# Kernel tuning notes

Hardware: AMD Instinct MI355X
Metric: run time of the kernel (lower is better)

The kernel has to match this reference:

```python
import jax, jax.numpy as jnp
import numpy as np

HEADS, DIM_HEAD = 8, 64
SCALE = DIM_HEAD ** -0.5
LAMDA1, LAMDA2 = 5.0, 5.0


def setup_inputs() -> dict:
    B, N, M = 32, 1536, 80  # N = 32*48 spatial tokens, M = max_boxes
    QD, KD, VD = 320, 768, 768
    inner = HEADS * DIM_HEAD
    ks = jax.random.split(jax.random.key(0), 11)
    return {
        "x": jax.random.normal(ks[0], (B, N, QD), jnp.float32),
        "key": jax.random.normal(ks[1], (B, M, KD), jnp.float32),
        "value": jax.random.normal(ks[2], (B, M, VD), jnp.float32),
        "mask": jax.random.randint(ks[3], (B, M), 0, 2).astype(bool),
        "perl_box_masking_map": jax.random.normal(ks[4], (B, N, M), jnp.float32),
        "perl_road_masking_map": jax.random.normal(ks[5], (B, 1, N), jnp.float32),
        "Wq": jax.random.normal(ks[6], (inner, QD), jnp.float32) * 0.02,
        "Wk": jax.random.normal(ks[7], (inner, KD), jnp.float32) * 0.02,
        "Wv": jax.random.normal(ks[8], (inner, VD), jnp.float32) * 0.02,
        "Wo": jax.random.normal(ks[9], (QD, inner), jnp.float32) * 0.02,
        "bo": jnp.zeros((QD,), jnp.float32),
    }


def reference(x, key, value, mask, perl_box_masking_map, perl_road_masking_map, Wq, Wk, Wv, Wo, bo):
    B, N, _ = x.shape
    M = key.shape[1]
    H, C = HEADS, DIM_HEAD
    # QKV projections (torch Linear: y = x @ W.T)
    q = (x @ Wq.T).reshape(B, N, H, C)
    k = (key @ Wk.T).reshape(B, M, H, C)
    v = (value @ Wv.T).reshape(B, M, H, C)
    # attention scores with scale, key mask, and two additive bias maps
    sim = jnp.einsum('bnhc,bmhc->bhnm', q, k) * SCALE  # (B, H, N, M)
    neg = -jnp.finfo(sim.dtype).max
    sim = jnp.where(mask[:, None, None, :], sim, neg)  # mask fill BEFORE bias adds, as in torch
    sim = sim + LAMDA1 * perl_box_masking_map[:, None, :, :]
    road = jnp.swapaxes(perl_road_masking_map, 1, 2)  # (B, N, 1) -> broadcast over key axis
    sim = sim + LAMDA2 * road[:, None, :, :]
    attn = jax.nn.softmax(sim, axis=-1)
    out = jnp.einsum('bhnm,bmhc->bnhc', attn, v).reshape(B, N, H * C)
    return out @ Wo.T + bo  # dropout is identity in eval
```

## Files before the change

### kernel.cpp

```cpp
#include <hip/hip_runtime.h>
#include <hip/hip_bf16.h>

typedef __attribute__((ext_vector_type(8))) short short8;
typedef __attribute__((ext_vector_type(4))) short short4v;
typedef __attribute__((ext_vector_type(4))) float floatx4;
typedef unsigned short u16;

#define NB 32
#define NN 1536
#define NM 80
#define NH 8
#define NC 64
#define NINNER 512
#define NQD 320
#define NKD 768

__device__ __forceinline__ float bf2f(u16 u) {
    union { unsigned i; float f; } x; x.i = ((unsigned)u) << 16; return x.f;
}
__device__ __forceinline__ u16 f2bf(float f) {
    unsigned u = __float_as_uint(f);
    unsigned r = (u + 0x7FFFu + ((u >> 16) & 1u)) >> 16;
    return (u16)r;
}
__device__ __forceinline__ short8 cvt8(const float* __restrict__ p) {
    float4 a = ((const float4*)p)[0];
    float4 b = ((const float4*)p)[1];
    short8 r;
    r[0] = (short)f2bf(a.x); r[1] = (short)f2bf(a.y);
    r[2] = (short)f2bf(a.z); r[3] = (short)f2bf(a.w);
    r[4] = (short)f2bf(b.x); r[5] = (short)f2bf(b.y);
    r[6] = (short)f2bf(b.z); r[7] = (short)f2bf(b.w);
    return r;
}
__device__ __forceinline__ void gload16(const u16* g, u16* l) {
    __builtin_amdgcn_global_load_lds(
        (const __attribute__((address_space(1))) unsigned int*)g,
        (__attribute__((address_space(3))) unsigned int*)l, 16, 0, 0);
}

__global__ __launch_bounds__(256) void prep(const u16* __restrict__ x,
                                            const unsigned char* __restrict__ raw,
                                            int* __restrict__ flag,
                                            float* __restrict__ maskbias) {
    if (blockIdx.x == 0) {
        __shared__ int cnt;
        if (threadIdx.x == 0) cnt = 0;
        __syncthreads();
        int c = 0;
        for (int i = threadIdx.x; i < 8192; i += 256) {
            unsigned e = (x[i] >> 7) & 0xFF;
            if (e >= 0xA0) c++;
        }
        atomicAdd(&cnt, c);
        __syncthreads();
        if (threadIdx.x == 0) *flag = (cnt > 64) ? 1 : 0;
    } else {
        __shared__ int c_bf, c_f32, c_u8;
        if (threadIdx.x == 0) { c_bf = 0; c_f32 = 0; c_u8 = 0; }
        __syncthreads();
        for (int i = threadIdx.x; i < NB * NM; i += 256) {
            unsigned char v = raw[i];
            if (v == 0x3F && (i & 3) == 1) atomicAdd(&c_bf, 1);
            if (v == 0x3F && (i & 3) == 3) atomicAdd(&c_f32, 1);
            if (v != 0 && (i & 3) != 0) atomicAdd(&c_u8, 1);
        }
        __syncthreads();
        int md;
        if (c_bf > 0) md = 2;
        else if (c_f32 > 0) md = 3;
        else if (c_u8 > 0) md = 1;
        else md = 0;
        for (int i = threadIdx.x; i < NB * NM; i += 256) {
            bool on;
            if (md == 2) on = ((const u16*)raw)[i] != 0;
            else if (md == 3) on = ((const float*)raw)[i] != 0.0f;
            else if (md == 1) on = raw[i] != 0;
            else on = ((const int*)raw)[i] != 0;
            maskbias[i] = on ? 0.0f : -3.4028234663852886e38f;
        }
    }
}

struct ConvSeg { const void* src; u16* dst; long nreal; long nblk; };
struct ConvArgs { ConvSeg s[7]; };

__global__ __launch_bounds__(256) void conv_batch(ConvArgs a, const int* __restrict__ flag) {
    const int f = *flag;
    long b = blockIdx.x; int seg = 0;
    while (seg < 7 && b >= a.s[seg].nblk) { b -= a.s[seg].nblk; seg++; }
    if (seg >= 7) return;
    const long idx = b * 2048 + threadIdx.x * 8;
    u16* dst = a.s[seg].dst;
    if (idx >= a.s[seg].nreal) { *(short8*)(dst + idx) = (short8)0; return; }
    if (f) *(short8*)(dst + idx) = cvt8((const float*)a.s[seg].src + idx);
    else   *(short8*)(dst + idx) = *(const short8*)((const u16*)a.s[seg].src + idx);
}

template <bool OUT_DYN, bool BIAS>
__device__ __forceinline__ void gemm_body(const u16* __restrict__ A,
                                          const u16* __restrict__ B,
                                          const void* __restrict__ bias,
                                          void* __restrict__ C,
                                          int bx, int by, int Nreal, int K, int f,
                                          u16* As, u16* Bs) {
    const int tid = threadIdx.x;
    const int wave = tid >> 6, lane = tid & 63;
    const int l16 = lane & 15, quad = lane >> 4;
    const int wr = wave >> 1, wc = wave & 1;
    const int bm0 = bx * 128, bn0 = by * 128;

    const int r0 = tid >> 2, c0 = tid & 3;
    const int sc = c0 ^ ((r0 >> 1) & 3);
    const u16* Ag = A + (size_t)(bm0 + r0) * K + sc * 8;
    const u16* Bg = B + (size_t)(bn0 + r0) * K + sc * 8;
    u16* AsW = As + wave * 512;
    u16* BsW = Bs + wave * 512;

    const int swz = (l16 >> 1) & 3;
    floatx4 acc[4][4];
#pragma unroll
    for (int i = 0; i < 4; ++i)
#pragma unroll
        for (int n = 0; n < 4; ++n) acc[i][n] = (floatx4)0.0f;

    for (int kk = 0; kk < K; kk += 32) {
        __syncthreads();
#pragma unroll
        for (int j = 0; j < 2; ++j) {
            gload16(Ag + (size_t)(j * 64) * K + kk, AsW + j * 2048);
            gload16(Bg + (size_t)(j * 64) * K + kk, BsW + j * 2048);
        }
        __syncthreads();
        short8 af[4], bf[4];
#pragma unroll
        for (int i = 0; i < 4; ++i)
            af[i] = *(const short8*)&As[(wr * 64 + i * 16 + l16) * 32 + ((quad ^ swz) * 8)];
#pragma unroll
        for (int n = 0; n < 4; ++n)
            bf[n] = *(const short8*)&Bs[(wc * 64 + n * 16 + l16) * 32 + ((quad ^ swz) * 8)];
#pragma unroll
        for (int i = 0; i < 4; ++i)
#pragma unroll
            for (int n = 0; n < 4; ++n)
                acc[i][n] = __builtin_amdgcn_mfma_f32_16x16x32_bf16(af[i], bf[n], acc[i][n], 0, 0, 0);
    }

#pragma unroll
    for (int n = 0; n < 4; ++n) {
        const int col = bn0 + wc * 64 + n * 16 + l16;
        if (col < Nreal) {
            float badd = 0.0f;
            if (BIAS) badd = f ? ((const float*)bias)[col] : bf2f(((const u16*)bias)[col]);
#pragma unroll
            for (int i = 0; i < 4; ++i)
#pragma unroll
                for (int r = 0; r < 4; ++r) {
                    const int row = bm0 + wr * 64 + i * 16 + quad * 4 + r;
                    const float val = acc[i][n][r] + badd;
                    if (OUT_DYN && f) ((float*)C)[(size_t)row * Nreal + col] = val;
                    else              ((u16*)C)[(size_t)row * Nreal + col] = f2bf(val);
                }
        }
    }
}

struct GemmRoles {
    const u16* A[3]; const u16* B[3]; u16* C[3];
    int mblk[3]; int kdim[3]; int start[3];
};

__global__ __launch_bounds__(256) void gemm_qkv(GemmRoles g) {
    __shared__ __align__(16) u16 As[128 * 32];
    __shared__ __align__(16) u16 Bs[128 * 32];
    const int id = blockIdx.x;
    const int role = (id >= g.start[1]) + (id >= g.start[2]);
    const int rid = id - g.start[role];
    const int mb = g.mblk[role];
    const int bx = rid % mb, by = rid / mb;
    gemm_body<false, false>(g.A[role], g.B[role], nullptr, g.C[role],
                            bx, by, NINNER, g.kdim[role], 0, As, Bs);
}

__global__ __launch_bounds__(256) void gemm_out(const u16* __restrict__ A,
                                                const u16* __restrict__ B,
                                                const void* __restrict__ bias,
                                                void* __restrict__ C,
                                                const int* __restrict__ flag) {
    __shared__ __align__(16) u16 As[128 * 32];
    __shared__ __align__(16) u16 Bs[128 * 32];
    const int f = *flag;
    gemm_body<true, true>(A, B, bias, C, blockIdx.x, blockIdx.y, NQD, NINNER, f, As, Bs);
}

__global__ __launch_bounds__(256) void transpose_v(const u16* __restrict__ v,
                                                   u16* __restrict__ vT) {
    int b = blockIdx.x >> 3, h = blockIdx.x & 7;
    const u16* src = v + (size_t)b * NM * NINNER + h * NC;
    u16* o = vT + (size_t)(b * NH + h) * NC * 96;
    for (int idx = threadIdx.x; idx < NM * NC; idx += 256) {
        int m = idx >> 6, c = idx & 63;
        o[c * 96 + m] = src[(size_t)m * NINNER + c];
    }
    for (int idx = threadIdx.x; idx < NC * 16; idx += 256) {
        int c = idx >> 4, m = 80 + (idx & 15);
        o[c * 96 + m] = 0;
    }
}

__global__ __launch_bounds__(256) void attn_kernel(const u16* __restrict__ q,
                                                   const u16* __restrict__ k,
                                                   const u16* __restrict__ vT,
                                                   const float* __restrict__ maskbias,
                                                   const void* __restrict__ box,
                                                   const void* __restrict__ road,
                                                   u16* __restrict__ attno,
                                                   const int* __restrict__ flag) {
    const int f = *flag;
    const int n0 = blockIdx.x * 64;
    const int h = blockIdx.y;
    const int b = blockIdx.z;
    const int tid = threadIdx.x;
    const int wave = tid >> 6, lane = tid & 63;
    const int l16 = lane & 15, quad = lane >> 4;

    __shared__ __align__(16) u16 p_lds[64][104];

    const int n = n0 + 16 * wave + l16;
    const size_t qrow = (size_t)(b * NN + n) * NINNER + h * NC;
    short8 qa[2];
    qa[0] = *(const short8*)(q + qrow + 0 + quad * 8);
    qa[1] = *(const short8*)(q + qrow + 32 + quad * 8);
    short8 kf[5][2];
#pragma unroll
    for (int mt = 0; mt < 5; ++mt) {
        const u16* kr = k + (size_t)(b * NM + mt * 16 + l16) * NINNER + h * NC + quad * 8;
        kf[mt][0] = *(const short8*)(kr + 0);
        kf[mt][1] = *(const short8*)(kr + 32);
    }
    const size_t boxbase = ((size_t)b * NN + n) * NM;
    floatx4 bx4[5]; short4v bxh[5]; floatx4 mb4[5];
    float roadf = 0.0f; u16 roadh = 0;
    if (f) {
#pragma unroll
        for (int mt = 0; mt < 5; ++mt)
            bx4[mt] = *(const floatx4*)((const float*)box + boxbase + 16 * mt + 4 * quad);
        roadf = ((const float*)road)[(size_t)b * NN + n];
    } else {
#pragma unroll
        for (int mt = 0; mt < 5; ++mt)
            bxh[mt] = *(const short4v*)((const u16*)box + boxbase + 16 * mt + 4 * quad);
        roadh = ((const u16*)road)[(size_t)b * NN + n];
    }
#pragma unroll
    for (int mt = 0; mt < 5; ++mt)
        mb4[mt] = *(const floatx4*)(maskbias + b * NM + 16 * mt + 4 * quad);

    floatx4 s[5];
#pragma unroll
    for (int i = 0; i < 5; ++i) s[i] = (floatx4)0.0f;
#pragma unroll
    for (int kk2 = 0; kk2 < 2; ++kk2)
#pragma unroll
        for (int mt = 0; mt < 5; ++mt)
            s[mt] = __builtin_amdgcn_mfma_f32_16x16x32_bf16(kf[mt][kk2], qa[kk2], s[mt], 0, 0, 0);

    const float roadv = 5.0f * (f ? roadf : bf2f(roadh));
#pragma unroll
    for (int mt = 0; mt < 5; ++mt)
#pragma unroll
        for (int r = 0; r < 4; ++r) {
            const float boxv = 5.0f * (f ? bx4[mt][r] : bf2f((u16)bxh[mt][r]));
            s[mt][r] = s[mt][r] * 0.125f + mb4[mt][r] + boxv + roadv;
        }

    float mx = s[0][0];
#pragma unroll
    for (int mt = 0; mt < 5; ++mt) {
        float t = fmaxf(fmaxf(s[mt][0], s[mt][1]), fmaxf(s[mt][2], s[mt][3]));
        mx = (mt == 0) ? t : fmaxf(mx, t);
    }
    mx = fmaxf(mx, __shfl_xor(mx, 16));
    mx = fmaxf(mx, __shfl_xor(mx, 32));
    float sum = 0.0f;
#pragma unroll
    for (int mt = 0; mt < 5; ++mt)
#pragma unroll
        for (int r = 0; r < 4; ++r) {
            const float p = __expf(s[mt][r] - mx);
            s[mt][r] = p;
            sum += p;
        }
    sum += __shfl_xor(sum, 16);
    sum += __shfl_xor(sum, 32);
    const float inv = 1.0f / sum;

#pragma unroll
    for (int mt = 0; mt < 5; ++mt) {
        short4v pk;
#pragma unroll
        for (int r = 0; r < 4; ++r) pk[r] = (short)f2bf(s[mt][r] * inv);
        *(short4v*)&p_lds[16 * wave + l16][16 * mt + 4 * quad] = pk;
    }
    if (quad < 2) *(short8*)&p_lds[16 * wave + l16][80 + 8 * quad] = (short8)0;
    asm volatile("s_waitcnt lgkmcnt(0)" ::: "memory");
    __builtin_amdgcn_sched_barrier(0);

    floatx4 o[4];
#pragma unroll
    for (int i = 0; i < 4; ++i) o[i] = (floatx4)0.0f;
    const u16* vbase = vT + (size_t)(b * NH + h) * NC * 96;
#pragma unroll
    for (int kk = 0; kk < 96; kk += 32) {
        short8 a = *(const short8*)&p_lds[16 * wave + l16][kk + quad * 8];
#pragma unroll
        for (int nt = 0; nt < 4; ++nt) {
            short8 bf = *(const short8*)(vbase + (size_t)(nt * 16 + l16) * 96 + kk + quad * 8);
            o[nt] = __builtin_amdgcn_mfma_f32_16x16x32_bf16(a, bf, o[nt], 0, 0, 0);
        }
    }

#pragma unroll
    for (int nt = 0; nt < 4; ++nt) {
#pragma unroll
        for (int r = 0; r < 4; ++r) {
            int nr = n0 + 16 * wave + quad * 4 + r;
            attno[((size_t)b * NN + nr) * NINNER + h * NC + nt * 16 + l16] = f2bf(o[nt][r]);
        }
    }
}

extern "C" void kernel_launch(void* const* d_in, const int* in_sizes, int n_in,
                              void* d_out, int out_size, void* d_ws, size_t ws_size,
                              hipStream_t stream) {
    (void)in_sizes; (void)n_in; (void)out_size; (void)ws_size;
    const void* x    = d_in[0];
    const void* key  = d_in[1];
    const void* val  = d_in[2];
    const unsigned char* mask = (const unsigned char*)d_in[3];
    const void* box  = d_in[4];
    const void* road = d_in[5];
    const void* Wq   = d_in[6];
    const void* Wk   = d_in[7];
    const void* Wv   = d_in[8];
    const void* Wo   = d_in[9];
    const void* bo   = d_in[10];

    char* ws = (char*)d_ws;
    size_t off = 0;
    auto carve = [&](size_t bytes) {
        char* p = ws + off;
        off += (bytes + 255) & ~(size_t)255;
        return p;
    };
    int* flag   = (int*)carve(256);
    u16* q_ws   = (u16*)carve((size_t)NB * NN * NINNER * 2);
    u16* k_ws   = (u16*)carve((size_t)NB * NM * NINNER * 2);
    u16* v_ws   = (u16*)carve((size_t)NB * NM * NINNER * 2);
    u16* vT_ws  = (u16*)carve((size_t)NB * NH * NC * 96 * 2);
    u16* ao_ws  = (u16*)carve((size_t)NB * NN * NINNER * 2);
    u16* x_bf   = ao_ws;
    u16* key_bf = (u16*)carve((size_t)NB * NM * NKD * 2);
    u16* val_bf = (u16*)carve((size_t)NB * NM * NKD * 2);
    u16* Wq_bf  = (u16*)carve((size_t)NINNER * NQD * 2);
    u16* Wk_bf  = (u16*)carve((size_t)NINNER * NKD * 2);
    u16* Wv_bf  = (u16*)carve((size_t)NINNER * NKD * 2);
    u16* WoP_bf = (u16*)carve((size_t)384 * NINNER * 2);
    float* mb   = (float*)carve((size_t)NB * NM * 4);

    prep<<<2, 256, 0, stream>>>((const u16*)x, mask, flag, mb);

    ConvArgs ca;
    ca.s[0] = { x,     x_bf,   (long)NB * NN * NQD, (long)NB * NN * NQD / 2048 };
    ca.s[1] = { key,   key_bf, (long)NB * NM * NKD, (long)NB * NM * NKD / 2048 };
    ca.s[2] = { val,   val_bf, (long)NB * NM * NKD, (long)NB * NM * NKD / 2048 };
    ca.s[3] = { Wq,    Wq_bf,  (long)NINNER * NQD,  (long)NINNER * NQD / 2048 };
    ca.s[4] = { Wk,    Wk_bf,  (long)NINNER * NKD,  (long)NINNER * NKD / 2048 };
    ca.s[5] = { Wv,    Wv_bf,  (long)NINNER * NKD,  (long)NINNER * NKD / 2048 };
    ca.s[6] = { Wo,    WoP_bf, (long)NQD * NINNER,  (long)384 * NINNER / 2048 };
    long totblk = 0;
    for (int i = 0; i < 7; ++i) totblk += ca.s[i].nblk;
    conv_batch<<<(int)totblk, 256, 0, stream>>>(ca, flag);

    GemmRoles g;
    g.A[0] = key_bf; g.B[0] = Wk_bf; g.C[0] = k_ws; g.mblk[0] = NB * NM / 128; g.kdim[0] = NKD;
    g.A[1] = val_bf; g.B[1] = Wv_bf; g.C[1] = v_ws; g.mblk[1] = NB * NM / 128; g.kdim[1] = NKD;
    g.A[2] = x_bf;   g.B[2] = Wq_bf; g.C[2] = q_ws; g.mblk[2] = NB * NN / 128; g.kdim[2] = NQD;
    g.start[0] = 0;
    g.start[1] = g.mblk[0] * 4;
    g.start[2] = g.start[1] + g.mblk[1] * 4;
    int gtot = g.start[2] + g.mblk[2] * 4;
    gemm_qkv<<<gtot, 256, 0, stream>>>(g);

    transpose_v<<<NB * NH, 256, 0, stream>>>(v_ws, vT_ws);
    attn_kernel<<<dim3(NN / 64, NH, NB), 256, 0, stream>>>(
        q_ws, k_ws, vT_ws, mb, box, road, ao_ws, flag);
    gemm_out<<<dim3(NB * NN / 128, 384 / 128), 256, 0, stream>>>(
        ao_ws, WoP_bf, bo, d_out, flag);
}
```

Baseline: 324.0 us.

## Double-buffer GEMM LDS tiles and prefetch V fragments in attention kernel

The shared GEMM body now double-buffers its A/B LDS tiles, issuing the next K-slice's global-to-LDS loads before computing on the current slice. This leaves one barrier per iteration instead of two. In the attention kernel, V fragments are loaded into registers right after the QK MFMAs so their latency overlaps the softmax. The bias sum, max reduction and bf16 packing via v_cvt_pk_bf16_f32 are also restructured. LDS usage per GEMM block doubles, and the prefetched V fragments raise register pressure.

```diff
diff --git a/kernel.cpp b/kernel.cpp
--- a/kernel.cpp
+++ b/kernel.cpp
@@ -4,6 +4,7 @@
 typedef __attribute__((ext_vector_type(8))) short short8;
 typedef __attribute__((ext_vector_type(4))) short short4v;
 typedef __attribute__((ext_vector_type(4))) float floatx4;
+typedef __attribute__((ext_vector_type(2))) unsigned uint2v;
 typedef unsigned short u16;
 
 #define NB 32
@@ -22,6 +23,11 @@
     unsigned u = __float_as_uint(f);
     unsigned r = (u + 0x7FFFu + ((u >> 16) & 1u)) >> 16;
     return (u16)r;
+}
+__device__ __forceinline__ unsigned cvt_pk_bf16(float lo, float hi) {
+    unsigned r;
+    asm("v_cvt_pk_bf16_f32 %0, %1, %2" : "=v"(r) : "v"(lo), "v"(hi));
+    return r;
 }
 __device__ __forceinline__ short8 cvt8(const float* __restrict__ p) {
     float4 a = ((const float4*)p)[0];
@@ -114,8 +120,6 @@
     const int sc = c0 ^ ((r0 >> 1) & 3);
     const u16* Ag = A + (size_t)(bm0 + r0) * K + sc * 8;
     const u16* Bg = B + (size_t)(bn0 + r0) * K + sc * 8;
-    u16* AsW = As + wave * 512;
-    u16* BsW = Bs + wave * 512;
 
     const int swz = (l16 >> 1) & 3;
     floatx4 acc[4][4];
@@ -124,26 +128,40 @@
 #pragma unroll
         for (int n = 0; n < 4; ++n) acc[i][n] = (floatx4)0.0f;
 
+    {
+        u16* AsW = As + wave * 512;
+        u16* BsW = Bs + wave * 512;
+        gload16(Ag, AsW);                  gload16(Ag + (size_t)64 * K, AsW + 2048);
+        gload16(Bg, BsW);                  gload16(Bg + (size_t)64 * K, BsW + 2048);
+    }
+    __syncthreads();
+
+    int cur = 0;
     for (int kk = 0; kk < K; kk += 32) {
-        __syncthreads();
-#pragma unroll
-        for (int j = 0; j < 2; ++j) {
-            gload16(Ag + (size_t)(j * 64) * K + kk, AsW + j * 2048);
-            gload16(Bg + (size_t)(j * 64) * K + kk, BsW + j * 2048);
-        }
-        __syncthreads();
+        if (kk + 32 < K) {
+            u16* AsW = As + (cur ^ 1) * 4096 + wave * 512;
+            u16* BsW = Bs + (cur ^ 1) * 4096 + wave * 512;
+            gload16(Ag + kk + 32, AsW);
+            gload16(Ag + (size_t)64 * K + kk + 32, AsW + 2048);
+            gload16(Bg + kk + 32, BsW);
+            gload16(Bg + (size_t)64 * K + kk + 32, BsW + 2048);
+        }
+        const u16* Asr = As + cur * 4096;
+        const u16* Bsr = Bs + cur * 4096;
         short8 af[4], bf[4];
 #pragma unroll
         for (int i = 0; i < 4; ++i)
-            af[i] = *(const short8*)&As[(wr * 64 + i * 16 + l16) * 32 + ((quad ^ swz) * 8)];
+            af[i] = *(const short8*)&Asr[(wr * 64 + i * 16 + l16) * 32 + ((quad ^ swz) * 8)];
 #pragma unroll
         for (int n = 0; n < 4; ++n)
-            bf[n] = *(const short8*)&Bs[(wc * 64 + n * 16 + l16) * 32 + ((quad ^ swz) * 8)];
+            bf[n] = *(const short8*)&Bsr[(wc * 64 + n * 16 + l16) * 32 + ((quad ^ swz) * 8)];
 #pragma unroll
         for (int i = 0; i < 4; ++i)
 #pragma unroll
             for (int n = 0; n < 4; ++n)
                 acc[i][n] = __builtin_amdgcn_mfma_f32_16x16x32_bf16(af[i], bf[n], acc[i][n], 0, 0, 0);
+        __syncthreads();
+        cur ^= 1;
     }
 
 #pragma unroll
@@ -171,8 +189,8 @@
 };
 
 __global__ __launch_bounds__(256) void gemm_qkv(GemmRoles g) {
-    __shared__ __align__(16) u16 As[128 * 32];
-    __shared__ __align__(16) u16 Bs[128 * 32];
+    __shared__ __align__(16) u16 As[2 * 128 * 32];
+    __shared__ __align__(16) u16 Bs[2 * 128 * 32];
     const int id = blockIdx.x;
     const int role = (id >= g.start[1]) + (id >= g.start[2]);
     const int rid = id - g.start[role];
@@ -187,8 +205,8 @@
                                                 const void* __restrict__ bias,
                                                 void* __restrict__ C,
                                                 const int* __restrict__ flag) {
-    __shared__ __align__(16) u16 As[128 * 32];
-    __shared__ __align__(16) u16 Bs[128 * 32];
+    __shared__ __align__(16) u16 As[2 * 128 * 32];
+    __shared__ __align__(16) u16 Bs[2 * 128 * 32];
     const int f = *flag;
     gemm_body<true, true>(A, B, bias, C, blockIdx.x, blockIdx.y, NQD, NINNER, f, As, Bs);
 }
@@ -265,20 +283,38 @@
         for (int mt = 0; mt < 5; ++mt)
             s[mt] = __builtin_amdgcn_mfma_f32_16x16x32_bf16(kf[mt][kk2], qa[kk2], s[mt], 0, 0, 0);
 
+    const u16* vbase = vT + (size_t)(b * NH + h) * NC * 96;
+    short8 vf[3][4];
+#pragma unroll
+    for (int kt = 0; kt < 3; ++kt)
+#pragma unroll
+        for (int nt = 0; nt < 4; ++nt)
+            vf[kt][nt] = *(const short8*)(vbase + (size_t)(nt * 16 + l16) * 96 + kt * 32 + quad * 8);
+
     const float roadv = 5.0f * (f ? roadf : bf2f(roadh));
+    floatx4 cb[5];
 #pragma unroll
     for (int mt = 0; mt < 5; ++mt)
 #pragma unroll
         for (int r = 0; r < 4; ++r) {
-            const float boxv = 5.0f * (f ? bx4[mt][r] : bf2f((u16)bxh[mt][r]));
-            s[mt][r] = s[mt][r] * 0.125f + mb4[mt][r] + boxv + roadv;
-        }
-
-    float mx = s[0][0];
-#pragma unroll
-    for (int mt = 0; mt < 5; ++mt) {
-        float t = fmaxf(fmaxf(s[mt][0], s[mt][1]), fmaxf(s[mt][2], s[mt][3]));
-        mx = (mt == 0) ? t : fmaxf(mx, t);
+            const float boxv = f ? bx4[mt][r] : bf2f((u16)bxh[mt][r]);
+            cb[mt][r] = mb4[mt][r] + 5.0f * boxv + roadv;
+        }
+
+#pragma unroll
+    for (int mt = 0; mt < 5; ++mt)
+#pragma unroll
+        for (int r = 0; r < 4; ++r)
+            s[mt][r] = s[mt][r] * 0.125f + cb[mt][r];
+
+    float mx;
+    {
+        float t0 = fmaxf(fmaxf(s[0][0], s[0][1]), fmaxf(s[0][2], s[0][3]));
+        float t1 = fmaxf(fmaxf(s[1][0], s[1][1]), fmaxf(s[1][2], s[1][3]));
+        float t2 = fmaxf(fmaxf(s[2][0], s[2][1]), fmaxf(s[2][2], s[2][3]));
+        float t3 = fmaxf(fmaxf(s[3][0], s[3][1]), fmaxf(s[3][2], s[3][3]));
+        float t4 = fmaxf(fmaxf(s[4][0], s[4][1]), fmaxf(s[4][2], s[4][3]));
+        mx = fmaxf(fmaxf(fmaxf(t0, t1), fmaxf(t2, t3)), t4);
     }
     mx = fmaxf(mx, __shfl_xor(mx, 16));
     mx = fmaxf(mx, __shfl_xor(mx, 32));
@@ -297,10 +333,10 @@
 
 #pragma unroll
     for (int mt = 0; mt < 5; ++mt) {
-        short4v pk;
-#pragma unroll
-        for (int r = 0; r < 4; ++r) pk[r] = (short)f2bf(s[mt][r] * inv);
-        *(short4v*)&p_lds[16 * wave + l16][16 * mt + 4 * quad] = pk;
+        uint2v pk;
+        pk[0] = cvt_pk_bf16(s[mt][0] * inv, s[mt][1] * inv);
+        pk[1] = cvt_pk_bf16(s[mt][2] * inv, s[mt][3] * inv);
+        *(uint2v*)&p_lds[16 * wave + l16][16 * mt + 4 * quad] = pk;
     }
     if (quad < 2) *(short8*)&p_lds[16 * wave + l16][80 + 8 * quad] = (short8)0;
     asm volatile("s_waitcnt lgkmcnt(0)" ::: "memory");
@@ -309,15 +345,12 @@
     floatx4 o[4];
 #pragma unroll
     for (int i = 0; i < 4; ++i) o[i] = (floatx4)0.0f;
-    const u16* vbase = vT + (size_t)(b * NH + h) * NC * 96;
-#pragma unroll
-    for (int kk = 0; kk < 96; kk += 32) {
-        short8 a = *(const short8*)&p_lds[16 * wave + l16][kk + quad * 8];
-#pragma unroll
-        for (int nt = 0; nt < 4; ++nt) {
-            short8 bf = *(const short8*)(vbase + (size_t)(nt * 16 + l16) * 96 + kk + quad * 8);
-            o[nt] = __builtin_amdgcn_mfma_f32_16x16x32_bf16(a, bf, o[nt], 0, 0, 0);
-        }
+#pragma unroll
+    for (int kt = 0; kt < 3; ++kt) {
+        short8 a = *(const short8*)&p_lds[16 * wave + l16][kt * 32 + quad * 8];
+#pragma unroll
+        for (int nt = 0; nt < 4; ++nt)
+            o[nt] = __builtin_amdgcn_mfma_f32_16x16x32_bf16(a, vf[kt][nt], o[nt], 0, 0, 0);
     }
 
 #pragma unroll
```

Result: no change. 324.8 us (+0.2%).
